# Performance work log

Measured on AMD Instinct MI355X. Metric: run time of the kernel, lower is better.

The kernel has to match this reference:

```python
import jax, jax.numpy as jnp
import numpy as np

WINDOW = 15          # window_size from __init__
EPS = 1e-8           # torch cosine_similarity eps


def setup_inputs() -> dict:
    B, S, D, NSPK = 4, 4096, 128, 9
    key = jax.random.key(0)
    k1, k2, k3 = jax.random.split(key, 3)
    x = jax.random.normal(k1, (B, S, D), dtype=jnp.float32)
    qmask = jax.random.uniform(k2, (S, B, NSPK), dtype=jnp.float32)
    # realistic dialogue lengths: between S//2 and S
    dia_len = jax.random.randint(k3, (B,), S // 2, S + 1, dtype=jnp.int32)
    return {"x": x, "qmask": qmask, "dia_len": dia_len}


def reference(x, qmask, dia_len):
    # x: [B,S,D], qmask: [S,B,NSPK], dia_len: [B]
    B, S, _ = x.shape
    xs = jax.lax.stop_gradient(x)  # original detaches x before similarity
    norms = jnp.maximum(jnp.linalg.norm(xs, axis=-1, keepdims=True), EPS)
    xn = xs / norms
    # cosine similarity, clamped, mapped to angular weight in [0,1]
    cos = jnp.clip(jnp.einsum('bid,bjd->bij', xn, xn), -1.0, 1.0)
    w = 1.0 - jnp.arccos(cos) / jnp.pi                       # [B,S,S]

    idx = jnp.arange(S)
    win = jnp.abs(idx[:, None] - idx[None, :]) <= WINDOW     # [S,S]
    valid = idx[None, :] < dia_len[:, None]                  # [B,S]
    M = win[None, :, :] & valid[:, :, None] & valid[:, None, :]  # [B,S,S]

    speakers = jnp.argmax(qmask, axis=-1).T                  # [B,S]
    same = speakers[:, :, None] == speakers[:, None, :]      # [B,S,S]

    # count of same-speaker tokens inside window (includes i itself);
    # doubling applied only when count > 1
    cnt = jnp.sum(M & same, axis=-1)                         # [B,S]
    dbl = (cnt > 1)[:, :, None] & same                       # [B,S,S]

    adj = w * M.astype(w.dtype) * (1.0 + dbl.astype(w.dtype))

    # symmetric-ish degree normalization D^-1/2 A D^-1/2 (row-sum degrees)
    deg = adj.sum(axis=-1)
    deg = jnp.where(deg == 0, 1.0, deg)
    dinv = deg ** -0.5
    adj = dinv[:, :, None] * adj * dinv[:, None, :]
    return adj
```

## Files before the change

kernel.cpp:

```cpp
#include <hip/hip_runtime.h>
#include <math.h>

#define BB 4
#define SS 4096
#define DD 128
#define NSPK 9
#define WIN 15
#define EPSN 1e-8f
#define INV_PI 0.31830988618379067f

typedef float vfloat4 __attribute__((ext_vector_type(4)));

__global__ __launch_bounds__(256) void k_main(const float* __restrict__ x,
                                              const float* __restrict__ qmask,
                                              const int* __restrict__ dia_len,
                                              float* __restrict__ band,
                                              float* __restrict__ dinv,
                                              float* __restrict__ out) {
    int wid  = (blockIdx.x * blockDim.x + threadIdx.x) >> 6;
    int lane = threadIdx.x & 63;
    int half = lane >> 5;
    int hl   = lane & 31;

    int row = wid * 2 + half;
    int b   = row >> 12;
    int i   = row & (SS - 1);
    int len = dia_len[b];

    int  j     = i - WIN + hl;
    bool inr   = (hl < 31) && (j >= 0) && (j < SS);
    bool maskv = inr && (i < len) && (j < len);

    int sj = 0;
    if (inr) {
        const float* q = qmask + ((size_t)j * BB + b) * NSPK;
        float best = q[0];
        #pragma unroll
        for (int k = 1; k < NSPK; ++k) {
            float qv = q[k];
            if (qv > best) { best = qv; sj = k; }
        }
    }
    int si = __shfl(sj, (lane & 32) + WIN);
    bool same = inr && (sj == si);

    float dot = 0.f, nj2 = 0.f;
    if (maskv) {
        const float4* xi = (const float4*)(x + (size_t)row * DD);
        const float4* xj = (const float4*)(x + ((size_t)b * SS + j) * DD);
        float d0 = 0.f, d1 = 0.f, n0 = 0.f, n1 = 0.f;
        #pragma unroll
        for (int d = 0; d < DD / 8; ++d) {
            float4 a0 = xi[2 * d],     c0 = xj[2 * d];
            float4 a1 = xi[2 * d + 1], c1 = xj[2 * d + 1];
            d0 += a0.x * c0.x + a0.y * c0.y + a0.z * c0.z + a0.w * c0.w;
            d1 += a1.x * c1.x + a1.y * c1.y + a1.z * c1.z + a1.w * c1.w;
            n0 += c0.x * c0.x + c0.y * c0.y + c0.z * c0.z + c0.w * c0.w;
            n1 += c1.x * c1.x + c1.y * c1.y + c1.z * c1.z + c1.w * c1.w;
        }
        dot = d0 + d1;
        nj2 = n0 + n1;
    }
    float ni2 = __shfl(nj2, (lane & 32) + WIN);

    float aij = 0.f;
    if (maskv) {
        float ni = fmaxf(sqrtf(ni2), EPSN);
        float nj = fmaxf(sqrtf(nj2), EPSN);
        float c  = dot / (ni * nj);
        c = fminf(fmaxf(c, -1.f), 1.f);
        aij = 1.f - acosf(c) * INV_PI;
    }

    unsigned long long bal = __ballot(maskv && same);
    unsigned long long hm  = half ? 0xFFFFFFFF00000000ull : 0x00000000FFFFFFFFull;
    int cnt = __popcll(bal & hm);
    if (maskv && same && cnt > 1) aij *= 2.f;

    float deg = aij;
    #pragma unroll
    for (int off = 16; off; off >>= 1) deg += __shfl_xor(deg, off);

    band[(size_t)row * 32 + hl] = aij;
    if (hl == 0) {
        float dv = (deg == 0.f) ? 1.f : deg;
        dinv[row] = 1.0f / sqrtf(dv);
    }

    int rA = wid * 2, iA = rA & (SS - 1);
    int rB = rA + 1,  iB = rB & (SS - 1);
    int fsA = (iA - WIN < 0 ? 0 : iA - WIN) >> 2;
    int feA = (iA + WIN > SS - 1 ? SS - 1 : iA + WIN) >> 2;
    int fsB = (iB - WIN < 0 ? 0 : iB - WIN) >> 2;
    int feB = (iB + WIN > SS - 1 ? SS - 1 : iB + WIN) >> 2;

    vfloat4 z = (vfloat4)(0.f);
    vfloat4* oA = (vfloat4*)(out + (size_t)rA * SS);
    vfloat4* oB = (vfloat4*)(out + (size_t)rB * SS);
    #pragma unroll
    for (int it = 0; it < SS / 4 / 64; ++it) {
        int f = it * 64 + lane;
        if (f < fsA || f > feA) __builtin_nontemporal_store(z, oA + f);
        if (f < fsB || f > feB) __builtin_nontemporal_store(z, oB + f);
    }
}

__global__ __launch_bounds__(256) void k_bw(const float* __restrict__ band,
                                            const float* __restrict__ dinv,
                                            float* __restrict__ out) {
    int row  = (blockIdx.x * blockDim.x + threadIdx.x) >> 6;
    int lane = threadIdx.x & 63;
    if (row >= BB * SS) return;
    int b = row >> 12, i = row & (SS - 1);
    int j0 = i - WIN; if (j0 < 0) j0 = 0;
    int j1 = i + WIN; if (j1 > SS - 1) j1 = SS - 1;
    int fs = j0 >> 2, fe = j1 >> 2;

    int j = fs * 4 + lane;
    if (j > fe * 4 + 3) return;

    float v = 0.f;
    if (j >= j0 && j <= j1) {
        v = band[(size_t)row * 32 + (j - i + WIN)] * dinv[row] * dinv[b * SS + j];
    }
    __builtin_nontemporal_store(v, out + (size_t)row * SS + j);
}

extern "C" void kernel_launch(void* const* d_in, const int* in_sizes, int n_in,
                              void* d_out, int out_size, void* d_ws, size_t ws_size,
                              hipStream_t stream) {
    const float* x       = (const float*)d_in[0];
    const float* qmask   = (const float*)d_in[1];
    const int*   dia_len = (const int*)d_in[2];
    float* out = (float*)d_out;

    char* ws = (char*)d_ws;
    const size_t rows = (size_t)BB * SS;
    float* band = (float*)ws;
    float* dinv = (float*)(ws + rows * 32 * 4);

    k_main<<<(int)(rows / 2 * 64 / 256), 256, 0, stream>>>(x, qmask, dia_len,
                                                           band, dinv, out);
    k_bw  <<<(int)(rows * 64 / 256),     256, 0, stream>>>(band, dinv, out);
}
```

Measured before the change: 288.5 us.

## Move zero-fill of output into fill kernel, write full rows once

Zero-filling the off-band output used to happen inside the band kernel, with a second kernel then writing the band values. Now the band kernel computes only band and dinv, and the fill kernel writes every float4 of each output row once, putting either zeros or normalized band values. This removes the split between zero stores and band stores in different kernels. The cost is that the band kernel finishes quickly and the whole 268MB write lands in a single kernel with one wave per row.

```diff
diff --git a/kernel.cpp b/kernel.cpp
--- a/kernel.cpp
+++ b/kernel.cpp
@@ -11,12 +11,11 @@
 
 typedef float vfloat4 __attribute__((ext_vector_type(4)));
 
-__global__ __launch_bounds__(256) void k_main(const float* __restrict__ x,
+__global__ __launch_bounds__(256) void k_band(const float* __restrict__ x,
                                               const float* __restrict__ qmask,
                                               const int* __restrict__ dia_len,
                                               float* __restrict__ band,
-                                              float* __restrict__ dinv,
-                                              float* __restrict__ out) {
+                                              float* __restrict__ dinv) {
     int wid  = (blockIdx.x * blockDim.x + threadIdx.x) >> 6;
     int lane = threadIdx.x & 63;
     int half = lane >> 5;
@@ -86,44 +85,37 @@
         float dv = (deg == 0.f) ? 1.f : deg;
         dinv[row] = 1.0f / sqrtf(dv);
     }
-
-    int rA = wid * 2, iA = rA & (SS - 1);
-    int rB = rA + 1,  iB = rB & (SS - 1);
-    int fsA = (iA - WIN < 0 ? 0 : iA - WIN) >> 2;
-    int feA = (iA + WIN > SS - 1 ? SS - 1 : iA + WIN) >> 2;
-    int fsB = (iB - WIN < 0 ? 0 : iB - WIN) >> 2;
-    int feB = (iB + WIN > SS - 1 ? SS - 1 : iB + WIN) >> 2;
-
-    vfloat4 z = (vfloat4)(0.f);
-    vfloat4* oA = (vfloat4*)(out + (size_t)rA * SS);
-    vfloat4* oB = (vfloat4*)(out + (size_t)rB * SS);
-    #pragma unroll
-    for (int it = 0; it < SS / 4 / 64; ++it) {
-        int f = it * 64 + lane;
-        if (f < fsA || f > feA) __builtin_nontemporal_store(z, oA + f);
-        if (f < fsB || f > feB) __builtin_nontemporal_store(z, oB + f);
-    }
 }
 
-__global__ __launch_bounds__(256) void k_bw(const float* __restrict__ band,
-                                            const float* __restrict__ dinv,
-                                            float* __restrict__ out) {
+__global__ __launch_bounds__(256) void k_fill(const float* __restrict__ band,
+                                              const float* __restrict__ dinv,
+                                              float* __restrict__ out) {
     int row  = (blockIdx.x * blockDim.x + threadIdx.x) >> 6;
     int lane = threadIdx.x & 63;
-    if (row >= BB * SS) return;
     int b = row >> 12, i = row & (SS - 1);
     int j0 = i - WIN; if (j0 < 0) j0 = 0;
     int j1 = i + WIN; if (j1 > SS - 1) j1 = SS - 1;
     int fs = j0 >> 2, fe = j1 >> 2;
 
-    int j = fs * 4 + lane;
-    if (j > fe * 4 + 3) return;
+    float di = dinv[row];
+    const float* brow = band + (size_t)row * 32;
+    const float* dj   = dinv + (size_t)b * SS;
+    vfloat4* orow = (vfloat4*)(out + (size_t)row * SS);
 
-    float v = 0.f;
-    if (j >= j0 && j <= j1) {
-        v = band[(size_t)row * 32 + (j - i + WIN)] * dinv[row] * dinv[b * SS + j];
+    #pragma unroll
+    for (int it = 0; it < SS / 4 / 64; ++it) {
+        int f = it * 64 + lane;
+        vfloat4 v = (vfloat4)(0.f);
+        if (f >= fs && f <= fe) {
+            #pragma unroll
+            for (int c = 0; c < 4; ++c) {
+                int j = f * 4 + c;
+                if (j >= j0 && j <= j1)
+                    v[c] = brow[j - i + WIN] * di * dj[j];
+            }
+        }
+        __builtin_nontemporal_store(v, orow + f);
     }
-    __builtin_nontemporal_store(v, out + (size_t)row * SS + j);
 }
 
 extern "C" void kernel_launch(void* const* d_in, const int* in_sizes, int n_in,
@@ -139,7 +131,7 @@
     float* band = (float*)ws;
     float* dinv = (float*)(ws + rows * 32 * 4);
 
-    k_main<<<(int)(rows / 2 * 64 / 256), 256, 0, stream>>>(x, qmask, dia_len,
-                                                           band, dinv, out);
-    k_bw  <<<(int)(rows * 64 / 256),     256, 0, stream>>>(band, dinv, out);
+    k_band<<<(int)(rows / 2 * 64 / 256), 256, 0, stream>>>(x, qmask, dia_len,
+                                                           band, dinv);
+    k_fill<<<(int)(rows * 64 / 256),     256, 0, stream>>>(band, dinv, out);
 }
```

Result: slower. 305.5 us (+5.9%).
